# Kernel tuning notes

Measured on AMD Instinct MI355X. Metric: run time of the kernel, lower is better.

The kernel has to match this reference:

```python
import jax, jax.numpy as jnp
import numpy as np

B, S, H, L, D, DI = 4, 32, 8, 128, 512, 2048
EPS = 1e-6
TEMP = float(D) ** 0.5


def layer_norm(x, g, b):
    mu = jnp.mean(x, axis=-1, keepdims=True)
    var = jnp.mean((x - mu) ** 2, axis=-1, keepdims=True)
    return (x - mu) * jax.lax.rsqrt(var + EPS) * g + b


def setup_inputs() -> dict:
    key = jax.random.key(0)
    ks = jax.random.split(key, 8)
    x = jax.random.normal(ks[0], (B, S, L, D), jnp.float32)
    mask = jax.random.randint(ks[1], (B, S, L), 0, 2, jnp.int32)
    # learned params
    w = jax.random.normal(ks[2], (1, 1, H, L, D), jnp.float32) * (1.0 / np.sqrt(D))
    v_w = jax.random.normal(ks[3], (D, D), jnp.float32) * 0.02   # nn.Linear weight (out,in)
    ln_g = jnp.ones((D,), jnp.float32)
    ln_b = jnp.zeros((D,), jnp.float32)
    w1 = jax.random.normal(ks[4], (DI, D), jnp.float32) * 0.02
    b1 = jnp.zeros((DI,), jnp.float32)
    w2 = jax.random.normal(ks[5], (D, DI), jnp.float32) * 0.02
    b2 = jnp.zeros((D,), jnp.float32)
    fln_g = jnp.ones((D,), jnp.float32)
    fln_b = jnp.zeros((D,), jnp.float32)
    return {"x": x, "mask": mask, "w": w, "v_w": v_w, "ln_g": ln_g, "ln_b": ln_b,
            "w1": w1, "b1": b1, "w2": w2, "b2": b2, "fln_g": fln_g, "fln_b": fln_b}


def reference(x, mask, w, v_w, ln_g, ln_b, w1, b1, w2, b2, fln_g, fln_b):
    # attn logits: broadcast mul + reduce over d_model == einsum over d
    attn = jnp.einsum('bsld,hld->bshl', x, w[0, 0]) / TEMP           # (B,S,H,L)
    attn = jnp.where(mask[:, :, None, :] == 0, -1e9, attn)
    attn = jax.nn.softmax(attn, axis=-1)                              # dropout: eval mode
    v = jnp.einsum('bsld,ed->bsle', x, v_w)                           # Linear no bias: x @ W.T
    out = jnp.einsum('bsld,bshl->bshd', v, attn)                      # weighted sum readout
    out = layer_norm(out, ln_g, ln_b)
    # PositionwiseFeedForward with residual + LayerNorm
    h = jax.nn.relu(jnp.einsum('bshd,fd->bshf', out, w1) + b1)
    y = jnp.einsum('bshf,df->bshd', h, w2) + b2 + out
    y = layer_norm(y, fln_g, fln_b)
    return y, attn
```

## Files before the change

### kernel.cpp

```cpp
#include <hip/hip_runtime.h>
#include <hip/hip_bf16.h>

#define BB 4
#define SS 32
#define HH 8
#define LL 128
#define DD 512
#define DI 2048
#define EPSN 1e-6f
#define INV_TEMP 0.04419417382415922f

#define NLOGIT_BLK 4096
#define NCAST_GRAN ((DI*DD/4)*2 + (DD*DD/4))
#define NCAST_BLK (NCAST_GRAN / 256)

#define NROW (BB*SS*HH)
#define SLICE ((size_t)NROW * DD)

typedef __attribute__((ext_vector_type(8))) short short8;
typedef __attribute__((ext_vector_type(4))) float float4v;

static __device__ __forceinline__ unsigned short f2b(float f) {
  __hip_bfloat16 h = __float2bfloat16(f);
  return *(unsigned short*)&h;
}

static __device__ __forceinline__ size_t pk(int m, int k, int K) {
  return ((((size_t)(m >> 4) * (K >> 5) + (k >> 5)) * 4 + ((k >> 3) & 3)) * 16
          + (m & 15)) * 8 + (k & 7);
}

__global__ __launch_bounds__(256) void pre_kernel(
    const float* __restrict__ x, const int* __restrict__ mask,
    const float* __restrict__ w, const float* __restrict__ w1,
    const float* __restrict__ w2, const float* __restrict__ v_w,
    unsigned short* __restrict__ w1b, unsigned short* __restrict__ w2b,
    unsigned short* __restrict__ v_wb, float* __restrict__ logits) {
  int blk = blockIdx.x;
  if (blk < NLOGIT_BLK) {
    int wv = threadIdx.x >> 6, lane = threadIdx.x & 63;
    int p  = blk * 4 + wv;
    int bs = p >> 7, l = p & (LL - 1);

    const float4* xr = (const float4*)(x + ((size_t)bs * LL + l) * DD) + lane * 2;
    float4 x0 = xr[0], x1 = xr[1];

    float acc[HH];
#pragma unroll
    for (int h = 0; h < HH; ++h) {
      const float4* wr = (const float4*)(w + ((size_t)h * LL + l) * DD) + lane * 2;
      float4 w0 = wr[0], w1v = wr[1];
      acc[h] = x0.x * w0.x + x0.y * w0.y + x0.z * w0.z + x0.w * w0.w +
               x1.x * w1v.x + x1.y * w1v.y + x1.z * w1v.z + x1.w * w1v.w;
    }
#pragma unroll
    for (int off = 32; off > 0; off >>= 1) {
#pragma unroll
      for (int h = 0; h < HH; ++h) acc[h] += __shfl_xor(acc[h], off);
    }
    if (lane == 0) {
      int msk = mask[bs * LL + l];
#pragma unroll
      for (int h = 0; h < HH; ++h) {
        float lg = msk ? acc[h] * INV_TEMP : -1e9f;
        logits[((size_t)bs * HH + h) * LL + l] = lg;
      }
    }
  } else {
    const int n1 = (DI * DD) / 4;
    const int n2 = n1;
    int i = (blk - NLOGIT_BLK) * 256 + threadIdx.x;
    float4 v;
    unsigned short* dst;
    size_t base;
    if (i < n1) {
      v = ((const float4*)w1)[i];
      dst = w1b;
      base = pk(i >> 7, (i & 127) * 4, DD);
    } else if (i < n1 + n2) {
      int j = i - n1;
      v = ((const float4*)w2)[j];
      dst = w2b;
      base = pk(j >> 9, (j & 511) * 4, DI);
    } else {
      int j = i - n1 - n2;
      v = ((const float4*)v_w)[j];
      dst = v_wb;
      base = pk(j >> 7, (j & 127) * 4, DD);
    }
    dst[base + 0] = f2b(v.x);
    dst[base + 1] = f2b(v.y);
    dst[base + 2] = f2b(v.z);
    dst[base + 3] = f2b(v.w);
  }
}

__global__ __launch_bounds__(512) void xa_kernel(
    const float* __restrict__ x, const float* __restrict__ logits,
    float* __restrict__ attn_out, unsigned short* __restrict__ xab) {
  int bs = blockIdx.x >> 1, half = blockIdx.x & 1;
  int t = threadIdx.x, wv = t >> 6, lane = t & 63;

  __shared__ float sattn_t[LL][HH];
  __shared__ float sxa[2][HH][256];

  if (wv < 4) {
    for (int h = wv; h < HH; h += 4) {
      const float* lg = logits + ((size_t)bs * HH + h) * LL;
      float v0 = lg[lane], v1 = lg[lane + 64];
      float m = fmaxf(v0, v1);
#pragma unroll
      for (int off = 32; off > 0; off >>= 1) m = fmaxf(m, __shfl_xor(m, off));
      float e0 = __expf(v0 - m), e1 = __expf(v1 - m);
      float s = e0 + e1;
#pragma unroll
      for (int off = 32; off > 0; off >>= 1) s += __shfl_xor(s, off);
      float inv = 1.f / s;
      e0 *= inv; e1 *= inv;
      sattn_t[lane][h]      = e0;
      sattn_t[lane + 64][h] = e1;
      if (half == 0) {
        float* ao = attn_out + ((size_t)bs * HH + h) * LL;
        ao[lane]      = e0;
        ao[lane + 64] = e1;
      }
    }
  }
  __syncthreads();

  int col = t & 255, lseg = t >> 8;
  int e = half * 256 + col;
  const float* xb = x + (size_t)bs * LL * DD;
  float acc[HH];
#pragma unroll
  for (int h = 0; h < HH; ++h) acc[h] = 0.f;
  int l0 = lseg * 64;
  for (int l = l0; l < l0 + 64; ++l) {
    float xv = xb[(size_t)l * DD + e];
    float4 a0 = *(const float4*)&sattn_t[l][0];
    float4 a1 = *(const float4*)&sattn_t[l][4];
    acc[0] += a0.x * xv; acc[1] += a0.y * xv;
    acc[2] += a0.z * xv; acc[3] += a0.w * xv;
    acc[4] += a1.x * xv; acc[5] += a1.y * xv;
    acc[6] += a1.z * xv; acc[7] += a1.w * xv;
  }
#pragma unroll
  for (int h = 0; h < HH; ++h) sxa[lseg][h][col] = acc[h];
  __syncthreads();
  if (t < 256) {
#pragma unroll
    for (int h = 0; h < HH; ++h) {
      int m = bs * HH + h;
      xab[pk(m, e, DD)] = f2b(sxa[0][h][t] + sxa[1][h][t]);
    }
  }
}

__global__ __launch_bounds__(256) void gemm_v_kernel(
    const unsigned short* __restrict__ xab, const unsigned short* __restrict__ v_wb,
    float* __restrict__ vpart) {
  int blk = blockIdx.x;
  int nt = blk & 7, mt = (blk >> 3) & 15, kslice = blk >> 7;
  int wv = threadIdx.x >> 6, lane = threadIdx.x & 63;
  int lm = lane & 15, lq = lane >> 4;

  int m0 = mt * 64 + wv * 16;
  int n0 = nt * 64;
  const short8* A8 = (const short8*)xab + (size_t)(m0 >> 4) * 16 * 64;
  const short8* B8 = (const short8*)v_wb;

  float4v acc[4];
#pragma unroll
  for (int nf = 0; nf < 4; ++nf) acc[nf] = (float4v){0.f, 0.f, 0.f, 0.f};

#pragma unroll
  for (int ci = 0; ci < 4; ++ci) {
    int c = kslice * 4 + ci;
    short8 a = A8[(size_t)c * 64 + lane];
#pragma unroll
    for (int nf = 0; nf < 4; ++nf) {
      short8 b = B8[((size_t)((n0 >> 4) + nf) * 16 + c) * 64 + lane];
      acc[nf] = __builtin_amdgcn_mfma_f32_16x16x32_bf16(a, b, acc[nf], 0, 0, 0);
    }
  }

  float* outp = vpart + (size_t)kslice * SLICE;
#pragma unroll
  for (int nf = 0; nf < 4; ++nf) {
    int col = n0 + nf * 16 + lm;
#pragma unroll
    for (int r = 0; r < 4; ++r)
      outp[(size_t)(m0 + lq * 4 + r) * DD + col] = acc[nf][r];
  }
}

__global__ __launch_bounds__(256) void ln_mid_kernel(
    const float* __restrict__ vpart, const float* __restrict__ ln_g,
    const float* __restrict__ ln_b, float* __restrict__ o_ln,
    unsigned short* __restrict__ o_lnb) {
  int wv = threadIdx.x >> 6, lane = threadIdx.x & 63;
  int row = blockIdx.x * 4 + wv;

  const float* p0 = vpart + (size_t)row * DD;
  float vals[8];
  float sum = 0.f, sq = 0.f;
#pragma unroll
  for (int k = 0; k < 8; ++k) {
    int d = lane + 64 * k;
    float v = p0[d] + p0[SLICE + d] + p0[2 * SLICE + d] + p0[3 * SLICE + d];
    vals[k] = v;
    sum += v;
    sq += v * v;
  }
#pragma unroll
  for (int off = 32; off > 0; off >>= 1) {
    sum += __shfl_xor(sum, off);
    sq  += __shfl_xor(sq, off);
  }
  float mu  = sum * (1.f / DD);
  float var = sq * (1.f / DD) - mu * mu;
  float rs  = rsqrtf(var + EPSN);
  float* op = o_ln + (size_t)row * DD;
#pragma unroll
  for (int k = 0; k < 8; ++k) {
    int d = lane + 64 * k;
    float v = (vals[k] - mu) * rs * ln_g[d] + ln_b[d];
    op[d] = v;
    o_lnb[pk(row, d, DD)] = f2b(v);
  }
}

__global__ __launch_bounds__(256) void gemm1_kernel(
    const unsigned short* __restrict__ o_lnb, const unsigned short* __restrict__ w1b,
    const float* __restrict__ b1, unsigned short* __restrict__ h1b) {
  int blk = blockIdx.x;
  int nt = blk & 31, mt = blk >> 5;
  int wv = threadIdx.x >> 6, lane = threadIdx.x & 63;
  int lm = lane & 15, lq = lane >> 4;

  int m0 = mt * 64 + wv * 16;
  int n0 = nt * 64;
  const short8* A8 = (const short8*)o_lnb + (size_t)(m0 >> 4) * 16 * 64;
  const short8* B8 = (const short8*)w1b;

  float4v acc[4];
#pragma unroll
  for (int nf = 0; nf < 4; ++nf) acc[nf] = (float4v){0.f, 0.f, 0.f, 0.f};

#pragma unroll 4
  for (int c = 0; c < 16; ++c) {
    short8 a = A8[(size_t)c * 64 + lane];
#pragma unroll
    for (int nf = 0; nf < 4; ++nf) {
      short8 b = B8[((size_t)((n0 >> 4) + nf) * 16 + c) * 64 + lane];
      acc[nf] = __builtin_amdgcn_mfma_f32_16x16x32_bf16(a, b, acc[nf], 0, 0, 0);
    }
  }

#pragma unroll
  for (int nf = 0; nf < 4; ++nf) {
    int col = n0 + nf * 16 + lm;
    float bb = b1[col];
#pragma unroll
    for (int r = 0; r < 4; ++r) {
      int row = m0 + lq * 4 + r;
      h1b[pk(row, col, DI)] = f2b(fmaxf(acc[nf][r] + bb, 0.f));
    }
  }
}

__global__ __launch_bounds__(256) void gemm2_kernel(
    const unsigned short* __restrict__ h1b, const unsigned short* __restrict__ w2b,
    float* __restrict__ ypart) {
  int blk = blockIdx.x;
  int nt = blk & 7, mt = (blk >> 3) & 15, kslice = blk >> 7;
  int wv = threadIdx.x >> 6, lane = threadIdx.x & 63;
  int lm = lane & 15, lq = lane >> 4;

  int m0 = mt * 64 + wv * 16;
  int n0 = nt * 64;
  const short8* A8 = (const short8*)h1b + (size_t)(m0 >> 4) * 64 * 64;
  const short8* B8 = (const short8*)w2b;

  float4v acc[4];
#pragma unroll
  for (int nf = 0; nf < 4; ++nf) acc[nf] = (float4v){0.f, 0.f, 0.f, 0.f};

#pragma unroll 4
  for (int ci = 0; ci < 16; ++ci) {
    int c = kslice * 16 + ci;
    short8 a = A8[(size_t)c * 64 + lane];
#pragma unroll
    for (int nf = 0; nf < 4; ++nf) {
      short8 b = B8[((size_t)((n0 >> 4) + nf) * 64 + c) * 64 + lane];
      acc[nf] = __builtin_amdgcn_mfma_f32_16x16x32_bf16(a, b, acc[nf], 0, 0, 0);
    }
  }

  float* outp = ypart + (size_t)kslice * SLICE;
#pragma unroll
  for (int nf = 0; nf < 4; ++nf) {
    int col = n0 + nf * 16 + lm;
#pragma unroll
    for (int r = 0; r < 4; ++r)
      outp[(size_t)(m0 + lq * 4 + r) * DD + col] = acc[nf][r];
  }
}

__global__ __launch_bounds__(256) void ln_final_kernel(
    const float* __restrict__ ypart, const float* __restrict__ o_ln,
    const float* __restrict__ b2, const float* __restrict__ fln_g,
    const float* __restrict__ fln_b, float* __restrict__ y_out) {
  int wv = threadIdx.x >> 6, lane = threadIdx.x & 63;
  int row = blockIdx.x * 4 + wv;

  const float* p0 = ypart + (size_t)row * DD;
  const float* ol = o_ln + (size_t)row * DD;
  float vals[8];
  float sum = 0.f, sq = 0.f;
#pragma unroll
  for (int k = 0; k < 8; ++k) {
    int d = lane + 64 * k;
    float v = p0[d] + p0[SLICE + d] + p0[2 * SLICE + d] + p0[3 * SLICE + d] +
              b2[d] + ol[d];
    vals[k] = v;
    sum += v;
    sq += v * v;
  }
#pragma unroll
  for (int off = 32; off > 0; off >>= 1) {
    sum += __shfl_xor(sum, off);
    sq  += __shfl_xor(sq, off);
  }
  float mu  = sum * (1.f / DD);
  float var = sq * (1.f / DD) - mu * mu;
  float rs  = rsqrtf(var + EPSN);
  float* yo = y_out + (size_t)row * DD;
#pragma unroll
  for (int k = 0; k < 8; ++k) {
    int d = lane + 64 * k;
    yo[d] = (vals[k] - mu) * rs * fln_g[d] + fln_b[d];
  }
}

extern "C" void kernel_launch(void* const* d_in, const int* in_sizes, int n_in,
                              void* d_out, int out_size, void* d_ws, size_t ws_size,
                              hipStream_t stream) {
  const float* x     = (const float*)d_in[0];
  const int*   mask  = (const int*)d_in[1];
  const float* w     = (const float*)d_in[2];
  const float* v_w   = (const float*)d_in[3];
  const float* ln_g  = (const float*)d_in[4];
  const float* ln_b  = (const float*)d_in[5];
  const float* w1    = (const float*)d_in[6];
  const float* b1    = (const float*)d_in[7];
  const float* w2    = (const float*)d_in[8];
  const float* b2    = (const float*)d_in[9];
  const float* fln_g = (const float*)d_in[10];
  const float* fln_b = (const float*)d_in[11];

  float* y    = (float*)d_out;
  float* attn = y + (size_t)BB * SS * HH * DD;

  char* ws = (char*)d_ws;
  float*          o_ln   = (float*)(ws);
  unsigned short* o_lnb  = (unsigned short*)(ws + 2097152);
  unsigned short* w1b    = (unsigned short*)(ws + 3145728);
  unsigned short* w2b    = (unsigned short*)(ws + 5242880);
  unsigned short* h1b    = (unsigned short*)(ws + 7340032);
  float*          ypart  = (float*)(ws + 11534336);
  unsigned short* v_wb   = (unsigned short*)(ws + 19922944);
  unsigned short* xab    = (unsigned short*)(ws + 20447232);
  float*          vpart  = (float*)(ws + 21495808);
  float*          logits = (float*)(ws + 29884416);

  pre_kernel<<<NLOGIT_BLK + NCAST_BLK, 256, 0, stream>>>(
      x, mask, w, w1, w2, v_w, w1b, w2b, v_wb, logits);
  xa_kernel<<<BB * SS * 2, 512, 0, stream>>>(x, logits, attn, xab);
  gemm_v_kernel<<<512, 256, 0, stream>>>(xab, v_wb, vpart);
  ln_mid_kernel<<<256, 256, 0, stream>>>(vpart, ln_g, ln_b, o_ln, o_lnb);
  gemm1_kernel<<<512, 256, 0, stream>>>(o_lnb, w1b, b1, h1b);
  gemm2_kernel<<<512, 256, 0, stream>>>(h1b, w2b, ypart);
  ln_final_kernel<<<256, 256, 0, stream>>>(ypart, o_ln, b2, fln_g, fln_b, y);
}
```

Measured before the change: 155.1 us.

## Fuse V projection into attention-readout kernel and LayerNorm into first FFN GEMM

The attention-weighted sum kernel now computes the V projection directly on its 8x256 readout slice with MFMA, writing two K-partial slices instead of staging bf16 xa to global and running a separate GEMM. The first FFN GEMM kernel now sums the two partials, applies the mid LayerNorm, packs the result to bf16 in shared memory, and runs the GEMM from there. This removes two kernel launches and global round trips. In exchange, the LayerNorm is recomputed redundantly by each of the 32 N-tile blocks, and the fused V GEMM leaves half the MFMA rows idle (M=8 padded to 16).

```diff
diff --git a/kernel.cpp b/kernel.cpp
--- a/kernel.cpp
+++ b/kernel.cpp
@@ -95,14 +95,17 @@
   }
 }
 
-__global__ __launch_bounds__(512) void xa_kernel(
+__global__ __launch_bounds__(512) void xa_v_kernel(
     const float* __restrict__ x, const float* __restrict__ logits,
-    float* __restrict__ attn_out, unsigned short* __restrict__ xab) {
+    const unsigned short* __restrict__ v_wb, float* __restrict__ attn_out,
+    float* __restrict__ vpart) {
   int bs = blockIdx.x >> 1, half = blockIdx.x & 1;
   int t = threadIdx.x, wv = t >> 6, lane = t & 63;
+  int lm = lane & 15, lq = lane >> 4;
 
   __shared__ float sattn_t[LL][HH];
   __shared__ float sxa[2][HH][256];
+  __shared__ unsigned short sxap[2048];
 
   if (wv < 4) {
     for (int h = wv; h < HH; h += 4) {
@@ -131,140 +134,140 @@
   int col = t & 255, lseg = t >> 8;
   int e = half * 256 + col;
   const float* xb = x + (size_t)bs * LL * DD;
-  float acc[HH];
-#pragma unroll
-  for (int h = 0; h < HH; ++h) acc[h] = 0.f;
-  int l0 = lseg * 64;
-  for (int l = l0; l < l0 + 64; ++l) {
-    float xv = xb[(size_t)l * DD + e];
-    float4 a0 = *(const float4*)&sattn_t[l][0];
-    float4 a1 = *(const float4*)&sattn_t[l][4];
-    acc[0] += a0.x * xv; acc[1] += a0.y * xv;
-    acc[2] += a0.z * xv; acc[3] += a0.w * xv;
-    acc[4] += a1.x * xv; acc[5] += a1.y * xv;
-    acc[6] += a1.z * xv; acc[7] += a1.w * xv;
-  }
-#pragma unroll
-  for (int h = 0; h < HH; ++h) sxa[lseg][h][col] = acc[h];
+  {
+    float acc[HH];
+#pragma unroll
+    for (int h = 0; h < HH; ++h) acc[h] = 0.f;
+    int l0 = lseg * 64;
+    for (int l = l0; l < l0 + 64; ++l) {
+      float xv = xb[(size_t)l * DD + e];
+      float4 a0 = *(const float4*)&sattn_t[l][0];
+      float4 a1 = *(const float4*)&sattn_t[l][4];
+      acc[0] += a0.x * xv; acc[1] += a0.y * xv;
+      acc[2] += a0.z * xv; acc[3] += a0.w * xv;
+      acc[4] += a1.x * xv; acc[5] += a1.y * xv;
+      acc[6] += a1.z * xv; acc[7] += a1.w * xv;
+    }
+#pragma unroll
+    for (int h = 0; h < HH; ++h) sxa[lseg][h][col] = acc[h];
+  }
   __syncthreads();
   if (t < 256) {
-#pragma unroll
-    for (int h = 0; h < HH; ++h) {
-      int m = bs * HH + h;
-      xab[pk(m, e, DD)] = f2b(sxa[0][h][t] + sxa[1][h][t]);
-    }
-  }
-}
-
-__global__ __launch_bounds__(256) void gemm_v_kernel(
-    const unsigned short* __restrict__ xab, const unsigned short* __restrict__ v_wb,
-    float* __restrict__ vpart) {
-  int blk = blockIdx.x;
-  int nt = blk & 7, mt = (blk >> 3) & 15, kslice = blk >> 7;
-  int wv = threadIdx.x >> 6, lane = threadIdx.x & 63;
-  int lm = lane & 15, lq = lane >> 4;
-
-  int m0 = mt * 64 + wv * 16;
-  int n0 = nt * 64;
-  const short8* A8 = (const short8*)xab + (size_t)(m0 >> 4) * 16 * 64;
-  const short8* B8 = (const short8*)v_wb;
-
-  float4v acc[4];
-#pragma unroll
-  for (int nf = 0; nf < 4; ++nf) acc[nf] = (float4v){0.f, 0.f, 0.f, 0.f};
-
-#pragma unroll
-  for (int ci = 0; ci < 4; ++ci) {
-    int c = kslice * 4 + ci;
-    short8 a = A8[(size_t)c * 64 + lane];
-#pragma unroll
-    for (int nf = 0; nf < 4; ++nf) {
-      short8 b = B8[((size_t)((n0 >> 4) + nf) * 16 + c) * 64 + lane];
-      acc[nf] = __builtin_amdgcn_mfma_f32_16x16x32_bf16(a, b, acc[nf], 0, 0, 0);
-    }
-  }
-
-  float* outp = vpart + (size_t)kslice * SLICE;
-#pragma unroll
-  for (int nf = 0; nf < 4; ++nf) {
-    int col = n0 + nf * 16 + lm;
-#pragma unroll
-    for (int r = 0; r < 4; ++r)
-      outp[(size_t)(m0 + lq * 4 + r) * DD + col] = acc[nf][r];
-  }
-}
-
-__global__ __launch_bounds__(256) void ln_mid_kernel(
+    int c = t >> 5, q = (t >> 3) & 3, el = t & 7;
+#pragma unroll
+    for (int h = 0; h < HH; ++h)
+      sxap[(((c * 4 + q) * 8) + h) * 8 + el] = f2b(sxa[0][h][t] + sxa[1][h][t]);
+  }
+  __syncthreads();
+
+  {
+    const short8* B8 = (const short8*)v_wb;
+    float4v acc[4];
+#pragma unroll
+    for (int nf = 0; nf < 4; ++nf) acc[nf] = (float4v){0.f, 0.f, 0.f, 0.f};
+#pragma unroll
+    for (int c = 0; c < 8; ++c) {
+      short8 a = *(const short8*)&sxap[(((c * 4 + lq) * 8) + (lm & 7)) * 8];
+#pragma unroll
+      for (int nf = 0; nf < 4; ++nf) {
+        int np = wv * 4 + nf;
+        short8 b = B8[((size_t)np * 16 + half * 8 + c) * 64 + lane];
+        acc[nf] = __builtin_amdgcn_mfma_f32_16x16x32_bf16(a, b, acc[nf], 0, 0, 0);
+      }
+    }
+    if (lq < 2) {
+      float* outp = vpart + (size_t)half * SLICE;
+#pragma unroll
+      for (int nf = 0; nf < 4; ++nf) {
+        int cc = wv * 64 + nf * 16 + lm;
+#pragma unroll
+        for (int r = 0; r < 4; ++r) {
+          int m = bs * HH + lq * 4 + r;
+          outp[(size_t)m * DD + cc] = acc[nf][r];
+        }
+      }
+    }
+  }
+}
+
+__global__ __launch_bounds__(256) void g1_kernel(
     const float* __restrict__ vpart, const float* __restrict__ ln_g,
-    const float* __restrict__ ln_b, float* __restrict__ o_ln,
-    unsigned short* __restrict__ o_lnb) {
-  int wv = threadIdx.x >> 6, lane = threadIdx.x & 63;
-  int row = blockIdx.x * 4 + wv;
-
-  const float* p0 = vpart + (size_t)row * DD;
-  float vals[8];
-  float sum = 0.f, sq = 0.f;
-#pragma unroll
-  for (int k = 0; k < 8; ++k) {
-    int d = lane + 64 * k;
-    float v = p0[d] + p0[SLICE + d] + p0[2 * SLICE + d] + p0[3 * SLICE + d];
-    vals[k] = v;
-    sum += v;
-    sq += v * v;
-  }
-#pragma unroll
-  for (int off = 32; off > 0; off >>= 1) {
-    sum += __shfl_xor(sum, off);
-    sq  += __shfl_xor(sq, off);
-  }
-  float mu  = sum * (1.f / DD);
-  float var = sq * (1.f / DD) - mu * mu;
-  float rs  = rsqrtf(var + EPSN);
-  float* op = o_ln + (size_t)row * DD;
-#pragma unroll
-  for (int k = 0; k < 8; ++k) {
-    int d = lane + 64 * k;
-    float v = (vals[k] - mu) * rs * ln_g[d] + ln_b[d];
-    op[d] = v;
-    o_lnb[pk(row, d, DD)] = f2b(v);
-  }
-}
-
-__global__ __launch_bounds__(256) void gemm1_kernel(
-    const unsigned short* __restrict__ o_lnb, const unsigned short* __restrict__ w1b,
-    const float* __restrict__ b1, unsigned short* __restrict__ h1b) {
+    const float* __restrict__ ln_b, const unsigned short* __restrict__ w1b,
+    const float* __restrict__ b1, float* __restrict__ o_ln,
+    unsigned short* __restrict__ h1b) {
   int blk = blockIdx.x;
   int nt = blk & 31, mt = blk >> 5;
   int wv = threadIdx.x >> 6, lane = threadIdx.x & 63;
   int lm = lane & 15, lq = lane >> 4;
 
-  int m0 = mt * 64 + wv * 16;
-  int n0 = nt * 64;
-  const short8* A8 = (const short8*)o_lnb + (size_t)(m0 >> 4) * 16 * 64;
-  const short8* B8 = (const short8*)w1b;
-
-  float4v acc[4];
-#pragma unroll
-  for (int nf = 0; nf < 4; ++nf) acc[nf] = (float4v){0.f, 0.f, 0.f, 0.f};
-
+  __shared__ unsigned short sA[64 * 512];
+
+  {
+    const float* gg = ln_g + lane * 8;
+    const float* gb = ln_b + lane * 8;
+    float g0 = gg[0], g1v = gg[1], g2 = gg[2], g3 = gg[3];
+    float g4 = gg[4], g5 = gg[5], g6 = gg[6], g7 = gg[7];
+    float bb0 = gb[0], bb1 = gb[1], bb2 = gb[2], bb3 = gb[3];
+    float bb4 = gb[4], bb5 = gb[5], bb6 = gb[6], bb7 = gb[7];
+    for (int i = 0; i < 16; ++i) {
+      int row = mt * 64 + wv * 16 + i;
+      const float* p0 = vpart + (size_t)row * DD + lane * 8;
+      float4 a0 = *(const float4*)p0;
+      float4 a1 = *(const float4*)(p0 + 4);
+      float4 c0 = *(const float4*)(p0 + SLICE);
+      float4 c1 = *(const float4*)(p0 + SLICE + 4);
+      float v0 = a0.x + c0.x, v1 = a0.y + c0.y, v2 = a0.z + c0.z, v3 = a0.w + c0.w;
+      float v4 = a1.x + c1.x, v5 = a1.y + c1.y, v6 = a1.z + c1.z, v7 = a1.w + c1.w;
+      float sum = v0 + v1 + v2 + v3 + v4 + v5 + v6 + v7;
+      float sq  = v0*v0 + v1*v1 + v2*v2 + v3*v3 + v4*v4 + v5*v5 + v6*v6 + v7*v7;
+#pragma unroll
+      for (int off = 32; off > 0; off >>= 1) {
+        sum += __shfl_xor(sum, off);
+        sq  += __shfl_xor(sq, off);
+      }
+      float mu  = sum * (1.f / DD);
+      float var = sq * (1.f / DD) - mu * mu;
+      float rs  = rsqrtf(var + EPSN);
+      float y0 = (v0 - mu) * rs * g0 + bb0, y1 = (v1 - mu) * rs * g1v + bb1;
+      float y2 = (v2 - mu) * rs * g2 + bb2, y3 = (v3 - mu) * rs * g3 + bb3;
+      float y4 = (v4 - mu) * rs * g4 + bb4, y5 = (v5 - mu) * rs * g5 + bb5;
+      float y6 = (v6 - mu) * rs * g6 + bb6, y7 = (v7 - mu) * rs * g7 + bb7;
+      unsigned short* d = &sA[((((wv * 16 + (lane >> 2)) * 4 + (lane & 3)) * 16) + i) * 8];
+      d[0] = f2b(y0); d[1] = f2b(y1); d[2] = f2b(y2); d[3] = f2b(y3);
+      d[4] = f2b(y4); d[5] = f2b(y5); d[6] = f2b(y6); d[7] = f2b(y7);
+      if (nt == 0) {
+        float* op = o_ln + (size_t)row * DD + lane * 8;
+        *(float4*)op = (float4){y0, y1, y2, y3};
+        *(float4*)(op + 4) = (float4){y4, y5, y6, y7};
+      }
+    }
+  }
+  __syncthreads();
+
+  {
+    const short8* B8 = (const short8*)w1b;
+    float4v acc[4];
+#pragma unroll
+    for (int nf = 0; nf < 4; ++nf) acc[nf] = (float4v){0.f, 0.f, 0.f, 0.f};
 #pragma unroll 4
-  for (int c = 0; c < 16; ++c) {
-    short8 a = A8[(size_t)c * 64 + lane];
+    for (int c = 0; c < 16; ++c) {
+      short8 a = *(const short8*)&sA[((((wv * 16 + c) * 4 + lq) * 16) + lm) * 8];
+#pragma unroll
+      for (int nf = 0; nf < 4; ++nf) {
+        int np = nt * 4 + nf;
+        short8 b = B8[((size_t)np * 16 + c) * 64 + lane];
+        acc[nf] = __builtin_amdgcn_mfma_f32_16x16x32_bf16(a, b, acc[nf], 0, 0, 0);
+      }
+    }
 #pragma unroll
     for (int nf = 0; nf < 4; ++nf) {
-      short8 b = B8[((size_t)((n0 >> 4) + nf) * 16 + c) * 64 + lane];
-      acc[nf] = __builtin_amdgcn_mfma_f32_16x16x32_bf16(a, b, acc[nf], 0, 0, 0);
-    }
-  }
-
-#pragma unroll
-  for (int nf = 0; nf < 4; ++nf) {
-    int col = n0 + nf * 16 + lm;
-    float bb = b1[col];
-#pragma unroll
-    for (int r = 0; r < 4; ++r) {
-      int row = m0 + lq * 4 + r;
-      h1b[pk(row, col, DI)] = f2b(fmaxf(acc[nf][r] + bb, 0.f));
+      int col = nt * 64 + nf * 16 + lm;
+      float bb = b1[col];
+#pragma unroll
+      for (int r = 0; r < 4; ++r) {
+        int row = mt * 64 + wv * 16 + lq * 4 + r;
+        h1b[pk(row, col, DI)] = f2b(fmaxf(acc[nf][r] + bb, 0.f));
+      }
     }
   }
 }
@@ -364,22 +367,18 @@
 
   char* ws = (char*)d_ws;
   float*          o_ln   = (float*)(ws);
-  unsigned short* o_lnb  = (unsigned short*)(ws + 2097152);
-  unsigned short* w1b    = (unsigned short*)(ws + 3145728);
-  unsigned short* w2b    = (unsigned short*)(ws + 5242880);
-  unsigned short* h1b    = (unsigned short*)(ws + 7340032);
-  float*          ypart  = (float*)(ws + 11534336);
-  unsigned short* v_wb   = (unsigned short*)(ws + 19922944);
-  unsigned short* xab    = (unsigned short*)(ws + 20447232);
-  float*          vpart  = (float*)(ws + 21495808);
-  float*          logits = (float*)(ws + 29884416);
+  unsigned short* w1b    = (unsigned short*)(ws + 2097152);
+  unsigned short* w2b    = (unsigned short*)(ws + 4194304);
+  unsigned short* h1b    = (unsigned short*)(ws + 6291456);
+  float*          ypart  = (float*)(ws + 10485760);
+  unsigned short* v_wb   = (unsigned short*)(ws + 18874368);
+  float*          vpart  = (float*)(ws + 19398656);
+  float*          logits = (float*)(ws + 23592960);
 
   pre_kernel<<<NLOGIT_BLK + NCAST_BLK, 256, 0, stream>>>(
       x, mask, w, w1, w2, v_w, w1b, w2b, v_wb, logits);
-  xa_kernel<<<BB * SS * 2, 512, 0, stream>>>(x, logits, attn, xab);
-  gemm_v_kernel<<<512, 256, 0, stream>>>(xab, v_wb, vpart);
-  ln_mid_kernel<<<256, 256, 0, stream>>>(vpart, ln_g, ln_b, o_ln, o_lnb);
-  gemm1_kernel<<<512, 256, 0, stream>>>(o_lnb, w1b, b1, h1b);
+  xa_v_kernel<<<BB * SS * 2, 512, 0, stream>>>(x, logits, v_wb, attn, vpart);
+  g1_kernel<<<512, 256, 0, stream>>>(vpart, ln_g, ln_b, w1b, b1, o_ln, h1b);
   gemm2_kernel<<<512, 256, 0, stream>>>(h1b, w2b, ypart);
   ln_final_kernel<<<256, 256, 0, stream>>>(ypart, o_ln, b2, fln_g, fln_b, y);
 }
```

Measured after the change: 158.9 us. 1.02x slower.
